# Kernel tuning notes

Measured on AMD Instinct MI355X. Metric: run time of the kernel, lower is better.

## Reference

```python
import jax, jax.numpy as jnp
import numpy as np

B, S, D = 8, 2048, 512
EPS = 1e-6
ROPE_THETA = 10000.0


def setup_inputs() -> dict:
    key = jax.random.key(0)
    ks = jax.random.split(key, 8)
    scale = 0.02
    return {
        "x": jax.random.normal(ks[0], (B, S, D), dtype=jnp.float32),
        "conv_w": jax.random.normal(ks[1], (D, D, 3), dtype=jnp.float32) * scale,
        "conv_b": jnp.zeros((D,), dtype=jnp.float32),
        "pre_g": jnp.ones((D,), dtype=jnp.float32),
        "q_g": jnp.ones((D,), dtype=jnp.float32),
        "k_g": jnp.ones((D,), dtype=jnp.float32),
        "Wq": jax.random.normal(ks[2], (D, D), dtype=jnp.float32) * scale,
        "Wk": jax.random.normal(ks[3], (D, D), dtype=jnp.float32) * scale,
        "Wv": jax.random.normal(ks[4], (D, D), dtype=jnp.float32) * scale,
    }


def _rmsnorm(x, g, eps=EPS):
    ms = jnp.mean(jnp.square(x), axis=-1, keepdims=True)
    return x * jax.lax.rsqrt(ms + eps) * g


def _rope_tables(seq_len, head_dim, dtype=jnp.float32):
    inv = 1.0 / (ROPE_THETA ** (jnp.arange(0, head_dim, 2, dtype=dtype) / head_dim))
    freqs = jnp.arange(seq_len, dtype=dtype)[:, None] * inv[None, :]  # [S, D/2]
    return jnp.cos(freqs), jnp.sin(freqs)


def _apply_rope(x, cos, sin):
    # x: [B, S, D]; treat last dim as D/2 complex pairs (interleaved real/imag)
    b, s, d = x.shape
    xr = x.reshape(b, s, d // 2, 2)
    x0, x1 = xr[..., 0], xr[..., 1]
    c = cos[None, :, :]
    sn = sin[None, :, :]
    o0 = x0 * c - x1 * sn
    o1 = x0 * sn + x1 * c
    return jnp.stack([o0, o1], axis=-1).reshape(b, s, d)


def reference(x, conv_w, conv_b, pre_g, q_g, k_g, Wq, Wk, Wv):
    b, s, d = x.shape
    # Conv1d over sequence axis (kernel 3, padding 1)
    xc = jnp.transpose(x, (0, 2, 1))  # [B, D, S]
    xc = jax.lax.conv_general_dilated(
        xc, conv_w, window_strides=(1,), padding=[(1, 1)],
        dimension_numbers=("NCH", "OIH", "NCH"))
    xc = xc + conv_b[None, :, None]
    x_norm = _rmsnorm(jnp.transpose(xc, (0, 2, 1)), pre_g)  # [B, S, D]

    q = _rmsnorm(jnp.einsum("bsd,ed->bse", x_norm, Wq), q_g)
    k = _rmsnorm(jnp.einsum("bsd,ed->bse", x_norm, Wk), k_g)
    v = jnp.einsum("bsd,ed->bse", x_norm, Wv)

    cos, sin = _rope_tables(s, d, x.dtype)
    q = _apply_rope(q, cos, sin)
    k = _apply_rope(k, cos, sin)

    scores = jnp.einsum("bqd,bkd->bqk", q, k) / jnp.sqrt(jnp.asarray(d, x.dtype))
    w = jax.nn.softmax(scores, axis=-1)  # dropout is identity in eval mode
    attended = jnp.einsum("bqk,bkd->bqd", w, v)
    out = x + attended
    return out.mean(axis=1)  # [B, D]
```

## Files before the change

### kernel.cpp

```cpp
#include <hip/hip_runtime.h>
#include <math.h>

#define BB 8
#define SS 2048
#define DDIM 512
#define KC 1536
#define EPSV 1e-6f
#define SCALE 0.044194173824159216f
#define LDP  40
#define LDP2 72

typedef unsigned short ushort_t;
using short8 = __attribute__((ext_vector_type(8))) short;
using f32x4  = __attribute__((ext_vector_type(4))) float;

__device__ inline unsigned short f2bf(float f) {
    union { float f; unsigned int u; } v; v.f = f;
    unsigned int r = v.u + 0x7FFFu + ((v.u >> 16) & 1u);
    return (unsigned short)(r >> 16);
}
__device__ inline unsigned int packbf(float a, float b) {
    return (unsigned int)f2bf(a) | ((unsigned int)f2bf(b) << 16);
}
__device__ inline float bf2f(unsigned short s) {
    union { unsigned int u; float f; } v; v.u = ((unsigned int)s) << 16; return v.f;
}
__device__ inline short8 ldfrag(const ushort_t* s, int row, int ko) {
    return *reinterpret_cast<const short8*>(&s[row * LDP + ko]);
}
__device__ inline short8 ldfrag2(const ushort_t* s, int row, int ko) {
    return *reinterpret_cast<const short8*>(&s[row * LDP2 + ko]);
}
__device__ inline uint4 lda_bc(const ushort_t* Ag, int s_, int ko) {
    return (s_ >= 0 && s_ < SS) ? *reinterpret_cast<const uint4*>(&Ag[(size_t)s_ * DDIM + ko])
                                : make_uint4(0, 0, 0, 0);
}

__global__ __launch_bounds__(256) void kx_cast(const float* __restrict__ x,
                                               ushort_t* __restrict__ xbf,
                                               float* __restrict__ xsum)
{
    const int t = threadIdx.x;
    const int b = blockIdx.y;
    const int r0 = blockIdx.x * 16;
    const int c0 = 2 * t;
    float s0 = 0.f, s1 = 0.f;
    for (int r = 0; r < 16; r++) {
        size_t row = (size_t)b * SS + r0 + r;
        float2 v = *reinterpret_cast<const float2*>(&x[row * DDIM + c0]);
        s0 += v.x; s1 += v.y;
        *reinterpret_cast<unsigned int*>(&xbf[row * DDIM + c0]) = packbf(v.x, v.y);
    }
    atomicAdd(&xsum[b * DDIM + c0], s0);
    atomicAdd(&xsum[b * DDIM + c0 + 1], s1);
}

__global__ __launch_bounds__(256) void k0_prep(
    const float* __restrict__ conv_w, const float* __restrict__ Wq,
    const float* __restrict__ Wk, const float* __restrict__ Wv,
    ushort_t* __restrict__ wcat, ushort_t* __restrict__ wqkv)
{
    int idx = blockIdx.x * 256 + threadIdx.x;
    {
        int o = idx / KC, kk = idx - o * KC;
        int t = kk >> 9, i = kk & 511;
        wcat[idx] = f2bf(conv_w[(size_t)o * KC + i * 3 + t]);
    }
    {
        int n = idx >> 9, d = idx & 511;
        const float* src = (n < 512) ? &Wq[(size_t)n * DDIM + d]
                         : (n < 1024) ? &Wk[(size_t)(n - 512) * DDIM + d]
                         : &Wv[(size_t)(n - 1024) * DDIM + d];
        wqkv[idx] = f2bf(*src);
    }
}

__global__ __launch_bounds__(256) void k1b_conv(
    const ushort_t* __restrict__ xbf, const ushort_t* __restrict__ wcat,
    const float* __restrict__ conv_b, ushort_t* __restrict__ ybf, float* __restrict__ rs)
{
    __shared__ ushort_t As[128 * LDP2];
    __shared__ ushort_t Bs[128 * LDP2];
    const int t = threadIdx.x;
    const int lane = t & 63, w = t >> 6;
    const int lm = lane & 15, lq = lane >> 4;
    const int wm = w >> 1, wn = w & 1;
    const int sr = t >> 3, sc = (t & 7) * 8;
    const int s0 = blockIdx.x * 128;
    const int n0 = blockIdx.y * 128;
    const int b  = blockIdx.z;
    const ushort_t* Ag = xbf + (size_t)b * SS * DDIM;
    const ushort_t* Bg = wcat + (size_t)n0 * KC;

    f32x4 acc[4][4];
    #pragma unroll
    for (int i = 0; i < 4; i++)
        #pragma unroll
        for (int j = 0; j < 4; j++) acc[i][j] = (f32x4){0.f, 0.f, 0.f, 0.f};

    uint4 ra0, ra1, ra2, ra3, rb0, rb1, rb2, rb3;
    #define LOADAB(dc) { \
        int tg_ = (dc) >> 3, ko_ = ((dc) & 7) * 64 + sc, kb_ = (dc) * 64 + sc; \
        int sa_ = s0 + sr + tg_ - 1; \
        ra0 = lda_bc(Ag, sa_,      ko_); ra1 = lda_bc(Ag, sa_ + 32, ko_); \
        ra2 = lda_bc(Ag, sa_ + 64, ko_); ra3 = lda_bc(Ag, sa_ + 96, ko_); \
        rb0 = *reinterpret_cast<const uint4*>(&Bg[(size_t)sr * KC + kb_]); \
        rb1 = *reinterpret_cast<const uint4*>(&Bg[(size_t)(sr + 32) * KC + kb_]); \
        rb2 = *reinterpret_cast<const uint4*>(&Bg[(size_t)(sr + 64) * KC + kb_]); \
        rb3 = *reinterpret_cast<const uint4*>(&Bg[(size_t)(sr + 96) * KC + kb_]); }

    LOADAB(0);
    for (int dc = 0; dc < 24; dc++) {
        *reinterpret_cast<uint4*>(&As[(sr)      * LDP2 + sc]) = ra0;
        *reinterpret_cast<uint4*>(&As[(sr + 32) * LDP2 + sc]) = ra1;
        *reinterpret_cast<uint4*>(&As[(sr + 64) * LDP2 + sc]) = ra2;
        *reinterpret_cast<uint4*>(&As[(sr + 96) * LDP2 + sc]) = ra3;
        *reinterpret_cast<uint4*>(&Bs[(sr)      * LDP2 + sc]) = rb0;
        *reinterpret_cast<uint4*>(&Bs[(sr + 32) * LDP2 + sc]) = rb1;
        *reinterpret_cast<uint4*>(&Bs[(sr + 64) * LDP2 + sc]) = rb2;
        *reinterpret_cast<uint4*>(&Bs[(sr + 96) * LDP2 + sc]) = rb3;
        __syncthreads();
        if (dc < 23) LOADAB(dc + 1);
        #pragma unroll
        for (int half = 0; half < 2; half++) {
            short8 af0 = ldfrag2(As, wm * 64 +  0 + lm, half * 32 + lq * 8);
            short8 af1 = ldfrag2(As, wm * 64 + 16 + lm, half * 32 + lq * 8);
            short8 af2 = ldfrag2(As, wm * 64 + 32 + lm, half * 32 + lq * 8);
            short8 af3 = ldfrag2(As, wm * 64 + 48 + lm, half * 32 + lq * 8);
            #pragma unroll
            for (int nt = 0; nt < 4; nt++) {
                short8 bfv = ldfrag2(Bs, wn * 64 + nt * 16 + lm, half * 32 + lq * 8);
                acc[0][nt] = __builtin_amdgcn_mfma_f32_16x16x32_bf16(af0, bfv, acc[0][nt], 0, 0, 0);
                acc[1][nt] = __builtin_amdgcn_mfma_f32_16x16x32_bf16(af1, bfv, acc[1][nt], 0, 0, 0);
                acc[2][nt] = __builtin_amdgcn_mfma_f32_16x16x32_bf16(af2, bfv, acc[2][nt], 0, 0, 0);
                acc[3][nt] = __builtin_amdgcn_mfma_f32_16x16x32_bf16(af3, bfv, acc[3][nt], 0, 0, 0);
            }
        }
        __syncthreads();
    }
    #undef LOADAB

    const int rbase = s0 + wm * 64;
    const int cbase = n0 + wn * 64;
    ushort_t* yb = ybf + (size_t)b * SS * DDIM;
    float* rsb = rs + (size_t)b * SS;
    float bias[4];
    #pragma unroll
    for (int nt = 0; nt < 4; nt++) bias[nt] = conv_b[cbase + nt * 16 + lm];
    #pragma unroll
    for (int mt = 0; mt < 4; mt++) {
        float pr[4] = {0.f, 0.f, 0.f, 0.f};
        #pragma unroll
        for (int nt = 0; nt < 4; nt++) {
            #pragma unroll
            for (int r = 0; r < 4; r++) {
                float val = acc[mt][nt][r] + bias[nt];
                yb[(size_t)(rbase + mt * 16 + lq * 4 + r) * DDIM + cbase + nt * 16 + lm] = f2bf(val);
                pr[r] = fmaf(val, val, pr[r]);
            }
        }
        #pragma unroll
        for (int r = 0; r < 4; r++) {
            float p = pr[r];
            p += __shfl_xor(p, 1, 64); p += __shfl_xor(p, 2, 64);
            p += __shfl_xor(p, 4, 64); p += __shfl_xor(p, 8, 64);
            if (lm == 0) atomicAdd(&rsb[rbase + mt * 16 + lq * 4 + r], p);
        }
    }
}

__global__ __launch_bounds__(256) void k1n_norm(
    const ushort_t* __restrict__ ybf, const float* __restrict__ rs,
    const float* __restrict__ pre_g, ushort_t* __restrict__ xnbf)
{
    const int t = threadIdx.x;
    const int b = blockIdx.y;
    const int r0 = blockIdx.x * 8;
    float2 pg = *reinterpret_cast<const float2*>(&pre_g[2 * t]);
    for (int r = 0; r < 8; r++) {
        size_t row = (size_t)b * SS + r0 + r;
        float inv = rsqrtf(rs[row] * (1.0f / DDIM) + EPSV);
        unsigned int yv = *reinterpret_cast<const unsigned int*>(&ybf[row * DDIM + 2 * t]);
        float v0 = bf2f((ushort_t)(yv & 0xFFFF)), v1 = bf2f((ushort_t)(yv >> 16));
        *reinterpret_cast<unsigned int*>(&xnbf[row * DDIM + 2 * t]) =
            packbf(v0 * inv * pg.x, v1 * inv * pg.y);
    }
}

__global__ __launch_bounds__(256) void k1c_qkv(
    const ushort_t* __restrict__ xnbf, const ushort_t* __restrict__ wqkv,
    ushort_t* __restrict__ qraw, ushort_t* __restrict__ kraw, ushort_t* __restrict__ vb,
    float* __restrict__ rq, float* __restrict__ rk)
{
    __shared__ ushort_t As[128 * LDP2];
    __shared__ ushort_t Bs[128 * LDP2];
    const int t = threadIdx.x;
    const int lane = t & 63, w = t >> 6;
    const int lm = lane & 15, lq = lane >> 4;
    const int wm = w >> 1, wn = w & 1;
    const int sr = t >> 3, sc = (t & 7) * 8;
    const int s0 = blockIdx.x * 128;
    const int n0 = blockIdx.y * 128;
    const int b  = blockIdx.z;
    const ushort_t* Ag = xnbf + ((size_t)b * SS + s0) * DDIM;
    const ushort_t* Bg = wqkv + (size_t)n0 * DDIM;

    f32x4 acc[4][4];
    #pragma unroll
    for (int i = 0; i < 4; i++)
        #pragma unroll
        for (int j = 0; j < 4; j++) acc[i][j] = (f32x4){0.f, 0.f, 0.f, 0.f};

    uint4 ra0, ra1, ra2, ra3, rb0, rb1, rb2, rb3;
    #define LOADAB2(dc) { \
        int ko_ = (dc) * 64 + sc; \
        ra0 = *reinterpret_cast<const uint4*>(&Ag[(size_t)sr * DDIM + ko_]); \
        ra1 = *reinterpret_cast<const uint4*>(&Ag[(size_t)(sr + 32) * DDIM + ko_]); \
        ra2 = *reinterpret_cast<const uint4*>(&Ag[(size_t)(sr + 64) * DDIM + ko_]); \
        ra3 = *reinterpret_cast<const uint4*>(&Ag[(size_t)(sr + 96) * DDIM + ko_]); \
        rb0 = *reinterpret_cast<const uint4*>(&Bg[(size_t)sr * DDIM + ko_]); \
        rb1 = *reinterpret_cast<const uint4*>(&Bg[(size_t)(sr + 32) * DDIM + ko_]); \
        rb2 = *reinterpret_cast<const uint4*>(&Bg[(size_t)(sr + 64) * DDIM + ko_]); \
        rb3 = *reinterpret_cast<const uint4*>(&Bg[(size_t)(sr + 96) * DDIM + ko_]); }

    LOADAB2(0);
    for (int dc = 0; dc < 8; dc++) {
        *reinterpret_cast<uint4*>(&As[(sr)      * LDP2 + sc]) = ra0;
        *reinterpret_cast<uint4*>(&As[(sr + 32) * LDP2 + sc]) = ra1;
        *reinterpret_cast<uint4*>(&As[(sr + 64) * LDP2 + sc]) = ra2;
        *reinterpret_cast<uint4*>(&As[(sr + 96) * LDP2 + sc]) = ra3;
        *reinterpret_cast<uint4*>(&Bs[(sr)      * LDP2 + sc]) = rb0;
        *reinterpret_cast<uint4*>(&Bs[(sr + 32) * LDP2 + sc]) = rb1;
        *reinterpret_cast<uint4*>(&Bs[(sr + 64) * LDP2 + sc]) = rb2;
        *reinterpret_cast<uint4*>(&Bs[(sr + 96) * LDP2 + sc]) = rb3;
        __syncthreads();
        if (dc < 7) LOADAB2(dc + 1);
        #pragma unroll
        for (int half = 0; half < 2; half++) {
            short8 af0 = ldfrag2(As, wm * 64 +  0 + lm, half * 32 + lq * 8);
            short8 af1 = ldfrag2(As, wm * 64 + 16 + lm, half * 32 + lq * 8);
            short8 af2 = ldfrag2(As, wm * 64 + 32 + lm, half * 32 + lq * 8);
            short8 af3 = ldfrag2(As, wm * 64 + 48 + lm, half * 32 + lq * 8);
            #pragma unroll
            for (int nt = 0; nt < 4; nt++) {
                short8 bfv = ldfrag2(Bs, wn * 64 + nt * 16 + lm, half * 32 + lq * 8);
                acc[0][nt] = __builtin_amdgcn_mfma_f32_16x16x32_bf16(af0, bfv, acc[0][nt], 0, 0, 0);
                acc[1][nt] = __builtin_amdgcn_mfma_f32_16x16x32_bf16(af1, bfv, acc[1][nt], 0, 0, 0);
                acc[2][nt] = __builtin_amdgcn_mfma_f32_16x16x32_bf16(af2, bfv, acc[2][nt], 0, 0, 0);
                acc[3][nt] = __builtin_amdgcn_mfma_f32_16x16x32_bf16(af3, bfv, acc[3][nt], 0, 0, 0);
            }
        }
        __syncthreads();
    }
    #undef LOADAB2

    const int which = blockIdx.y >> 2;
    const int rbase = s0 + wm * 64;
    const int cbase = ((blockIdx.y & 3) * 128) + wn * 64;
    if (which == 2) {
        ushort_t* vbb = vb + (size_t)b * SS * DDIM;
        #pragma unroll
        for (int mt = 0; mt < 4; mt++)
            #pragma unroll
            for (int nt = 0; nt < 4; nt++)
                #pragma unroll
                for (int r = 0; r < 4; r++)
                    vbb[(size_t)(rbase + mt * 16 + lq * 4 + r) * DDIM + cbase + nt * 16 + lm] =
                        f2bf(acc[mt][nt][r]);
    } else {
        ushort_t* db = (which ? kraw : qraw) + (size_t)b * SS * DDIM;
        float* rb = (which ? rk : rq) + (size_t)b * SS;
        #pragma unroll
        for (int mt = 0; mt < 4; mt++) {
            float pr[4] = {0.f, 0.f, 0.f, 0.f};
            #pragma unroll
            for (int nt = 0; nt < 4; nt++) {
                #pragma unroll
                for (int r = 0; r < 4; r++) {
                    float val = acc[mt][nt][r];
                    db[(size_t)(rbase + mt * 16 + lq * 4 + r) * DDIM + cbase + nt * 16 + lm] = f2bf(val);
                    pr[r] = fmaf(val, val, pr[r]);
                }
            }
            #pragma unroll
            for (int r = 0; r < 4; r++) {
                float p = pr[r];
                p += __shfl_xor(p, 1, 64); p += __shfl_xor(p, 2, 64);
                p += __shfl_xor(p, 4, 64); p += __shfl_xor(p, 8, 64);
                if (lm == 0) atomicAdd(&rb[rbase + mt * 16 + lq * 4 + r], p);
            }
        }
    }
}

__global__ __launch_bounds__(256) void k1d_rope(
    ushort_t* q_io, ushort_t* k_io,
    const float* __restrict__ rq, const float* __restrict__ rk,
    const float* __restrict__ q_g, const float* __restrict__ k_g)
{
    const int t = threadIdx.x;
    const int b = blockIdx.y;
    const int r0 = blockIdx.x * 8;
    const int c0 = 2 * t;
    float qg0 = q_g[c0], qg1 = q_g[c0 + 1];
    float kg0 = k_g[c0], kg1 = k_g[c0 + 1];
    float invf = (float)pow(10000.0, -(double)c0 / (double)DDIM);
    for (int r = 0; r < 8; r++) {
        int srow = r0 + r;
        size_t rowi = (size_t)b * SS + srow;
        float iq = rsqrtf(rq[rowi] * (1.0f / DDIM) + EPSV);
        float ik = rsqrtf(rk[rowi] * (1.0f / DDIM) + EPSV);
        size_t off = rowi * DDIM + c0;
        unsigned int qv = *reinterpret_cast<const unsigned int*>(&q_io[off]);
        unsigned int kv = *reinterpret_cast<const unsigned int*>(&k_io[off]);
        float q0 = bf2f((ushort_t)(qv & 0xFFFF)) * iq * qg0;
        float q1 = bf2f((ushort_t)(qv >> 16)) * iq * qg1;
        float k0v = bf2f((ushort_t)(kv & 0xFFFF)) * ik * kg0;
        float k1v = bf2f((ushort_t)(kv >> 16)) * ik * kg1;
        float ang = (float)srow * invf, sn, cs;
        sincosf(ang, &sn, &cs);
        *reinterpret_cast<unsigned int*>(&q_io[off]) = packbf(q0 * cs - q1 * sn, q0 * sn + q1 * cs);
        *reinterpret_cast<unsigned int*>(&k_io[off]) = packbf(k0v * cs - k1v * sn, k0v * sn + k1v * cs);
    }
}

__global__ __launch_bounds__(256, 4) void k2a_rowsum(
    const ushort_t* __restrict__ qb, const ushort_t* __restrict__ kb,
    ushort_t* __restrict__ P, float* __restrict__ l)
{
    __shared__ ushort_t As[128 * LDP];
    __shared__ ushort_t Bs[128 * LDP];
    const int t = threadIdx.x;
    const int lane = t & 63, w = t >> 6;
    const int lm = lane & 15, lq = lane >> 4;
    const int wm = w >> 1, wn = w & 1;
    const int srow = t >> 2, scol = (t & 3) * 8;
    const int b  = blockIdx.x;
    const int qt = blockIdx.y;
    const int kt = blockIdx.z;

    const ushort_t* Ag = qb + ((size_t)b * SS + qt * 128) * DDIM;
    const ushort_t* Bg = kb + ((size_t)b * SS + kt * 128) * DDIM;

    f32x4 acc[4][4];
    #pragma unroll
    for (int i = 0; i < 4; i++)
        #pragma unroll
        for (int j = 0; j < 4; j++) acc[i][j] = (f32x4){0.f, 0.f, 0.f, 0.f};

    uint4 ra0 = *reinterpret_cast<const uint4*>(&Ag[(size_t)srow * DDIM + scol]);
    uint4 ra1 = *reinterpret_cast<const uint4*>(&Ag[(size_t)(srow + 64) * DDIM + scol]);
    uint4 rb0 = *reinterpret_cast<const uint4*>(&Bg[(size_t)srow * DDIM + scol]);
    uint4 rb1 = *reinterpret_cast<const uint4*>(&Bg[(size_t)(srow + 64) * DDIM + scol]);

    for (int dc = 0; dc < 16; dc++) {
        *reinterpret_cast<uint4*>(&As[srow * LDP + scol]) = ra0;
        *reinterpret_cast<uint4*>(&As[(srow + 64) * LDP + scol]) = ra1;
        *reinterpret_cast<uint4*>(&Bs[srow * LDP + scol]) = rb0;
        *reinterpret_cast<uint4*>(&Bs[(srow + 64) * LDP + scol]) = rb1;
        __syncthreads();
        if (dc < 15) {
            int off = (dc + 1) * 32 + scol;
            ra0 = *reinterpret_cast<const uint4*>(&Ag[(size_t)srow * DDIM + off]);
            ra1 = *reinterpret_cast<const uint4*>(&Ag[(size_t)(srow + 64) * DDIM + off]);
            rb0 = *reinterpret_cast<const uint4*>(&Bg[(size_t)srow * DDIM + off]);
            rb1 = *reinterpret_cast<const uint4*>(&Bg[(size_t)(srow + 64) * DDIM + off]);
        }
        short8 af[4];
        #pragma unroll
        for (int mt = 0; mt < 4; mt++)
            af[mt] = ldfrag(As, wm * 64 + mt * 16 + lm, lq * 8);
        #pragma unroll
        for (int nt = 0; nt < 4; nt++) {
            short8 bfv = ldfrag(Bs, wn * 64 + nt * 16 + lm, lq * 8);
            #pragma unroll
            for (int mt = 0; mt < 4; mt++)
                acc[mt][nt] = __builtin_amdgcn_mfma_f32_16x16x32_bf16(af[mt], bfv, acc[mt][nt], 0, 0, 0);
        }
        __syncthreads();
    }

    const int rbase = qt * 128 + wm * 64;
    const int cbase = kt * 128 + wn * 64;
    ushort_t* Pb = P + (size_t)b * SS * SS;
    float* lrow = l + (size_t)b * SS;
    #pragma unroll
    for (int mt = 0; mt < 4; mt++) {
        #pragma unroll
        for (int r = 0; r < 4; r++) {
            const int row = rbase + mt * 16 + lq * 4 + r;
            float rowp = 0.f;
            #pragma unroll
            for (int nt = 0; nt < 4; nt++) {
                float e = __expf(acc[mt][nt][r] * SCALE);
                Pb[(size_t)row * SS + cbase + nt * 16 + lm] = f2bf(e);
                rowp += e;
            }
            float p = rowp;
            p += __shfl_xor(p, 1, 64); p += __shfl_xor(p, 2, 64);
            p += __shfl_xor(p, 4, 64); p += __shfl_xor(p, 8, 64);
            if (lm == 0) atomicAdd(&lrow[row], p);
        }
    }
}

__global__ __launch_bounds__(256) void k2c_colred(
    const ushort_t* __restrict__ P, const float* __restrict__ l,
    float* __restrict__ cw)
{
    const int t = threadIdx.x;
    const int b = blockIdx.z;
    const int k0 = blockIdx.x * 1024 + t * 4;
    const int q0 = blockIdx.y * 128;
    const ushort_t* Pb = P + ((size_t)b * SS + q0) * SS;
    const float* lb = l + (size_t)b * SS + q0;
    float a0 = 0.f, a1 = 0.f, a2 = 0.f, a3 = 0.f;
    for (int q = 0; q < 128; q++) {
        float rl = 1.0f / lb[q];
        uint2 pp = *reinterpret_cast<const uint2*>(&Pb[(size_t)q * SS + k0]);
        a0 = fmaf(bf2f((ushort_t)(pp.x & 0xFFFF)), rl, a0);
        a1 = fmaf(bf2f((ushort_t)(pp.x >> 16)), rl, a1);
        a2 = fmaf(bf2f((ushort_t)(pp.y & 0xFFFF)), rl, a2);
        a3 = fmaf(bf2f((ushort_t)(pp.y >> 16)), rl, a3);
    }
    atomicAdd(&cw[(size_t)b * SS + k0], a0);
    atomicAdd(&cw[(size_t)b * SS + k0 + 1], a1);
    atomicAdd(&cw[(size_t)b * SS + k0 + 2], a2);
    atomicAdd(&cw[(size_t)b * SS + k0 + 3], a3);
}

__global__ __launch_bounds__(256) void k4_out(
    const float* __restrict__ xsum, const ushort_t* __restrict__ v,
    const float* __restrict__ cwv, float* __restrict__ out)
{
    const int b = blockIdx.x, c = blockIdx.y;
    const int t = threadIdx.x;
    const int srow0 = c * (SS / 16);
    const ushort_t* vb = v + ((size_t)b * SS + srow0) * DDIM;
    const float* cwb   = cwv + (size_t)b * SS + srow0;
    float a0 = (c == 0) ? xsum[b * DDIM + t]       : 0.f;
    float a1 = (c == 0) ? xsum[b * DDIM + t + 256] : 0.f;
    for (int r = 0; r < SS / 16; r++) {
        float w = cwb[r];
        a0 += w * bf2f(vb[(size_t)r * DDIM + t]);
        a1 += w * bf2f(vb[(size_t)r * DDIM + t + 256]);
    }
    atomicAdd(&out[b * DDIM + t],       a0 * (1.0f / SS));
    atomicAdd(&out[b * DDIM + t + 256], a1 * (1.0f / SS));
}

extern "C" void kernel_launch(void* const* d_in, const int* in_sizes, int n_in,
                              void* d_out, int out_size, void* d_ws, size_t ws_size,
                              hipStream_t stream)
{
    const float* x      = (const float*)d_in[0];
    const float* conv_w = (const float*)d_in[1];
    const float* conv_b = (const float*)d_in[2];
    const float* pre_g  = (const float*)d_in[3];
    const float* q_g    = (const float*)d_in[4];
    const float* k_g    = (const float*)d_in[5];
    const float* Wq     = (const float*)d_in[6];
    const float* Wk     = (const float*)d_in[7];
    const float* Wv     = (const float*)d_in[8];
    float* out          = (float*)d_out;

    const size_t NTOK = (size_t)BB * SS * DDIM;
    char* p = (char*)d_ws;
    ushort_t* xbf = (ushort_t*)p; p += NTOK * 2;
    ushort_t* ybf = (ushort_t*)p; p += NTOK * 2;
    ushort_t* xn  = (ushort_t*)p; p += NTOK * 2;
                         p += NTOK * 2;
    ushort_t* qio = (ushort_t*)p; p += NTOK * 2;
    ushort_t* kio = (ushort_t*)p; p += NTOK * 2;
    ushort_t* vb  = (ushort_t*)p; p += NTOK * 2;
    ushort_t* wcat = (ushort_t*)p; p += (size_t)DDIM * KC * 2;
    ushort_t* wqkv = (ushort_t*)p; p += (size_t)KC * DDIM * 2;
    float* rs   = (float*)p; p += (size_t)BB * SS * 4;
    float* rq   = (float*)p; p += (size_t)BB * SS * 4;
    float* rk   = (float*)p; p += (size_t)BB * SS * 4;
    float* lbuf = (float*)p; p += (size_t)BB * SS * 4;
    float* cwb  = (float*)p; p += (size_t)BB * SS * 4;
    float* xsum = (float*)p; p += (size_t)BB * DDIM * 4;

    ushort_t* Pbuf = xbf;

    (void)hipMemsetAsync(d_out, 0, (size_t)out_size * sizeof(float), stream);
    (void)hipMemsetAsync(rs, 0, ((size_t)BB * SS * 5 + (size_t)BB * DDIM) * sizeof(float), stream);

    kx_cast<<<dim3(SS / 16, BB), 256, 0, stream>>>(x, xbf, xsum);
    k0_prep<<<dim3(DDIM * KC / 256), 256, 0, stream>>>(conv_w, Wq, Wk, Wv, wcat, wqkv);
    k1b_conv<<<dim3(SS / 128, 4, BB), 256, 0, stream>>>(xbf, wcat, conv_b, ybf, rs);
    k1n_norm<<<dim3(SS / 8, BB), 256, 0, stream>>>(ybf, rs, pre_g, xn);
    k1c_qkv<<<dim3(SS / 128, 12, BB), 256, 0, stream>>>(xn, wqkv, qio, kio, vb, rq, rk);
    k1d_rope<<<dim3(SS / 8, BB), 256, 0, stream>>>(qio, kio, rq, rk, q_g, k_g);
    k2a_rowsum<<<dim3(BB, SS / 128, SS / 128), 256, 0, stream>>>(qio, kio, Pbuf, lbuf);
    k2c_colred<<<dim3(SS / 1024, SS / 128, BB), 256, 0, stream>>>(Pbuf, lbuf, cwb);
    k4_out<<<dim3(BB, 16), 256, 0, stream>>>(xsum, vb, cwb, out);
}
```

Measured before the change: 283.8 us.

## Widen QK^T tile to 256 keys, vectorize cast and column-reduction kernels

The scores kernel now computes a 128x256 tile per block, reusing each Q fragment across two key halves and halving the number of Q reloads and row-sum atomics. Its occupancy hint is dropped because the accumulator count doubles. The column-reduction kernel switches to 16-byte loads with 8 columns per thread over 64-row query chunks. The cast kernel uses float4 loads and combines its two row halves in shared memory before issuing atomics. The larger tile raises register pressure and may lower occupancy.

```diff
diff --git a/kernel.cpp b/kernel.cpp
--- a/kernel.cpp
+++ b/kernel.cpp
@@ -40,19 +40,32 @@
                                                ushort_t* __restrict__ xbf,
                                                float* __restrict__ xsum)
 {
+    __shared__ float xr[512];
     const int t = threadIdx.x;
     const int b = blockIdx.y;
-    const int r0 = blockIdx.x * 16;
-    const int c0 = 2 * t;
-    float s0 = 0.f, s1 = 0.f;
-    for (int r = 0; r < 16; r++) {
+    const int half = t >> 7;
+    const int c0 = (t & 127) * 4;
+    const int r0 = blockIdx.x * 16 + half * 8;
+    float s0 = 0.f, s1 = 0.f, s2 = 0.f, s3 = 0.f;
+    for (int r = 0; r < 8; r++) {
         size_t row = (size_t)b * SS + r0 + r;
-        float2 v = *reinterpret_cast<const float2*>(&x[row * DDIM + c0]);
-        s0 += v.x; s1 += v.y;
-        *reinterpret_cast<unsigned int*>(&xbf[row * DDIM + c0]) = packbf(v.x, v.y);
-    }
-    atomicAdd(&xsum[b * DDIM + c0], s0);
-    atomicAdd(&xsum[b * DDIM + c0 + 1], s1);
+        float4 v = *reinterpret_cast<const float4*>(&x[row * DDIM + c0]);
+        s0 += v.x; s1 += v.y; s2 += v.z; s3 += v.w;
+        *reinterpret_cast<uint2*>(&xbf[row * DDIM + c0]) =
+            make_uint2(packbf(v.x, v.y), packbf(v.z, v.w));
+    }
+    if (half) {
+        float4* dst = reinterpret_cast<float4*>(&xr[(t - 128) * 4]);
+        *dst = make_float4(s0, s1, s2, s3);
+    }
+    __syncthreads();
+    if (!half) {
+        float4 o = *reinterpret_cast<const float4*>(&xr[t * 4]);
+        atomicAdd(&xsum[b * DDIM + c0],     s0 + o.x);
+        atomicAdd(&xsum[b * DDIM + c0 + 1], s1 + o.y);
+        atomicAdd(&xsum[b * DDIM + c0 + 2], s2 + o.z);
+        atomicAdd(&xsum[b * DDIM + c0 + 3], s3 + o.w);
+    }
 }
 
 __global__ __launch_bounds__(256) void k0_prep(
@@ -324,12 +337,12 @@
     }
 }
 
-__global__ __launch_bounds__(256, 4) void k2a_rowsum(
+__global__ __launch_bounds__(256) void k2a_rowsum(
     const ushort_t* __restrict__ qb, const ushort_t* __restrict__ kb,
     ushort_t* __restrict__ P, float* __restrict__ l)
 {
     __shared__ ushort_t As[128 * LDP];
-    __shared__ ushort_t Bs[128 * LDP];
+    __shared__ ushort_t Bs[256 * LDP];
     const int t = threadIdx.x;
     const int lane = t & 63, w = t >> 6;
     const int lm = lane & 15, lq = lane >> 4;
@@ -340,48 +353,63 @@
     const int kt = blockIdx.z;
 
     const ushort_t* Ag = qb + ((size_t)b * SS + qt * 128) * DDIM;
-    const ushort_t* Bg = kb + ((size_t)b * SS + kt * 128) * DDIM;
-
-    f32x4 acc[4][4];
+    const ushort_t* Bg = kb + ((size_t)b * SS + kt * 256) * DDIM;
+
+    f32x4 accA[4][4], accB[4][4];
     #pragma unroll
     for (int i = 0; i < 4; i++)
         #pragma unroll
-        for (int j = 0; j < 4; j++) acc[i][j] = (f32x4){0.f, 0.f, 0.f, 0.f};
-
-    uint4 ra0 = *reinterpret_cast<const uint4*>(&Ag[(size_t)srow * DDIM + scol]);
-    uint4 ra1 = *reinterpret_cast<const uint4*>(&Ag[(size_t)(srow + 64) * DDIM + scol]);
-    uint4 rb0 = *reinterpret_cast<const uint4*>(&Bg[(size_t)srow * DDIM + scol]);
-    uint4 rb1 = *reinterpret_cast<const uint4*>(&Bg[(size_t)(srow + 64) * DDIM + scol]);
-
+        for (int j = 0; j < 4; j++) {
+            accA[i][j] = (f32x4){0.f, 0.f, 0.f, 0.f};
+            accB[i][j] = (f32x4){0.f, 0.f, 0.f, 0.f};
+        }
+
+    uint4 qa0, qa1, kb0, kb1, kb2, kb3;
+    #define LOADQK(dc) { \
+        int ko_ = (dc) * 32 + scol; \
+        qa0 = *reinterpret_cast<const uint4*>(&Ag[(size_t)srow * DDIM + ko_]); \
+        qa1 = *reinterpret_cast<const uint4*>(&Ag[(size_t)(srow + 64) * DDIM + ko_]); \
+        kb0 = *reinterpret_cast<const uint4*>(&Bg[(size_t)srow * DDIM + ko_]); \
+        kb1 = *reinterpret_cast<const uint4*>(&Bg[(size_t)(srow + 64) * DDIM + ko_]); \
+        kb2 = *reinterpret_cast<const uint4*>(&Bg[(size_t)(srow + 128) * DDIM + ko_]); \
+        kb3 = *reinterpret_cast<const uint4*>(&Bg[(size_t)(srow + 192) * DDIM + ko_]); }
+
+    LOADQK(0);
     for (int dc = 0; dc < 16; dc++) {
-        *reinterpret_cast<uint4*>(&As[srow * LDP + scol]) = ra0;
-        *reinterpret_cast<uint4*>(&As[(srow + 64) * LDP + scol]) = ra1;
-        *reinterpret_cast<uint4*>(&Bs[srow * LDP + scol]) = rb0;
-        *reinterpret_cast<uint4*>(&Bs[(srow + 64) * LDP + scol]) = rb1;
+        *reinterpret_cast<uint4*>(&As[srow * LDP + scol]) = qa0;
+        *reinterpret_cast<uint4*>(&As[(srow + 64) * LDP + scol]) = qa1;
+        *reinterpret_cast<uint4*>(&Bs[srow * LDP + scol]) = kb0;
+        *reinterpret_cast<uint4*>(&Bs[(srow + 64) * LDP + scol]) = kb1;
+        *reinterpret_cast<uint4*>(&Bs[(srow + 128) * LDP + scol]) = kb2;
+        *reinterpret_cast<uint4*>(&Bs[(srow + 192) * LDP + scol]) = kb3;
         __syncthreads();
-        if (dc < 15) {
-            int off = (dc + 1) * 32 + scol;
-            ra0 = *reinterpret_cast<const uint4*>(&Ag[(size_t)srow * DDIM + off]);
-            ra1 = *reinterpret_cast<const uint4*>(&Ag[(size_t)(srow + 64) * DDIM + off]);
-            rb0 = *reinterpret_cast<const uint4*>(&Bg[(size_t)srow * DDIM + off]);
-            rb1 = *reinterpret_cast<const uint4*>(&Bg[(size_t)(srow + 64) * DDIM + off]);
-        }
-        short8 af[4];
-        #pragma unroll
-        for (int mt = 0; mt < 4; mt++)
-            af[mt] = ldfrag(As, wm * 64 + mt * 16 + lm, lq * 8);
+        if (dc < 15) LOADQK(dc + 1);
+        short8 af0 = ldfrag(As, wm * 64 +  0 + lm, lq * 8);
+        short8 af1 = ldfrag(As, wm * 64 + 16 + lm, lq * 8);
+        short8 af2 = ldfrag(As, wm * 64 + 32 + lm, lq * 8);
+        short8 af3 = ldfrag(As, wm * 64 + 48 + lm, lq * 8);
         #pragma unroll
         for (int nt = 0; nt < 4; nt++) {
             short8 bfv = ldfrag(Bs, wn * 64 + nt * 16 + lm, lq * 8);
-            #pragma unroll
-            for (int mt = 0; mt < 4; mt++)
-                acc[mt][nt] = __builtin_amdgcn_mfma_f32_16x16x32_bf16(af[mt], bfv, acc[mt][nt], 0, 0, 0);
+            accA[0][nt] = __builtin_amdgcn_mfma_f32_16x16x32_bf16(af0, bfv, accA[0][nt], 0, 0, 0);
+            accA[1][nt] = __builtin_amdgcn_mfma_f32_16x16x32_bf16(af1, bfv, accA[1][nt], 0, 0, 0);
+            accA[2][nt] = __builtin_amdgcn_mfma_f32_16x16x32_bf16(af2, bfv, accA[2][nt], 0, 0, 0);
+            accA[3][nt] = __builtin_amdgcn_mfma_f32_16x16x32_bf16(af3, bfv, accA[3][nt], 0, 0, 0);
+        }
+        #pragma unroll
+        for (int nt = 0; nt < 4; nt++) {
+            short8 bfv = ldfrag(Bs, 128 + wn * 64 + nt * 16 + lm, lq * 8);
+            accB[0][nt] = __builtin_amdgcn_mfma_f32_16x16x32_bf16(af0, bfv, accB[0][nt], 0, 0, 0);
+            accB[1][nt] = __builtin_amdgcn_mfma_f32_16x16x32_bf16(af1, bfv, accB[1][nt], 0, 0, 0);
+            accB[2][nt] = __builtin_amdgcn_mfma_f32_16x16x32_bf16(af2, bfv, accB[2][nt], 0, 0, 0);
+            accB[3][nt] = __builtin_amdgcn_mfma_f32_16x16x32_bf16(af3, bfv, accB[3][nt], 0, 0, 0);
         }
         __syncthreads();
     }
+    #undef LOADQK
 
     const int rbase = qt * 128 + wm * 64;
-    const int cbase = kt * 128 + wn * 64;
+    const int cbase = kt * 256 + wn * 64;
     ushort_t* Pb = P + (size_t)b * SS * SS;
     float* lrow = l + (size_t)b * SS;
     #pragma unroll
@@ -392,8 +420,14 @@
             float rowp = 0.f;
             #pragma unroll
             for (int nt = 0; nt < 4; nt++) {
-                float e = __expf(acc[mt][nt][r] * SCALE);
+                float e = __expf(accA[mt][nt][r] * SCALE);
                 Pb[(size_t)row * SS + cbase + nt * 16 + lm] = f2bf(e);
+                rowp += e;
+            }
+            #pragma unroll
+            for (int nt = 0; nt < 4; nt++) {
+                float e = __expf(accB[mt][nt][r] * SCALE);
+                Pb[(size_t)row * SS + cbase + 128 + nt * 16 + lm] = f2bf(e);
                 rowp += e;
             }
             float p = rowp;
@@ -409,24 +443,27 @@
     float* __restrict__ cw)
 {
     const int t = threadIdx.x;
-    const int b = blockIdx.z;
-    const int k0 = blockIdx.x * 1024 + t * 4;
-    const int q0 = blockIdx.y * 128;
+    const int b = blockIdx.y;
+    const int k0 = t * 8;
+    const int q0 = blockIdx.x * 64;
     const ushort_t* Pb = P + ((size_t)b * SS + q0) * SS;
     const float* lb = l + (size_t)b * SS + q0;
-    float a0 = 0.f, a1 = 0.f, a2 = 0.f, a3 = 0.f;
-    for (int q = 0; q < 128; q++) {
+    float a[8] = {0.f, 0.f, 0.f, 0.f, 0.f, 0.f, 0.f, 0.f};
+    for (int q = 0; q < 64; q++) {
         float rl = 1.0f / lb[q];
-        uint2 pp = *reinterpret_cast<const uint2*>(&Pb[(size_t)q * SS + k0]);
-        a0 = fmaf(bf2f((ushort_t)(pp.x & 0xFFFF)), rl, a0);
-        a1 = fmaf(bf2f((ushort_t)(pp.x >> 16)), rl, a1);
-        a2 = fmaf(bf2f((ushort_t)(pp.y & 0xFFFF)), rl, a2);
-        a3 = fmaf(bf2f((ushort_t)(pp.y >> 16)), rl, a3);
-    }
-    atomicAdd(&cw[(size_t)b * SS + k0], a0);
-    atomicAdd(&cw[(size_t)b * SS + k0 + 1], a1);
-    atomicAdd(&cw[(size_t)b * SS + k0 + 2], a2);
-    atomicAdd(&cw[(size_t)b * SS + k0 + 3], a3);
+        uint4 pp = *reinterpret_cast<const uint4*>(&Pb[(size_t)q * SS + k0]);
+        a[0] = fmaf(bf2f((ushort_t)(pp.x & 0xFFFF)), rl, a[0]);
+        a[1] = fmaf(bf2f((ushort_t)(pp.x >> 16)), rl, a[1]);
+        a[2] = fmaf(bf2f((ushort_t)(pp.y & 0xFFFF)), rl, a[2]);
+        a[3] = fmaf(bf2f((ushort_t)(pp.y >> 16)), rl, a[3]);
+        a[4] = fmaf(bf2f((ushort_t)(pp.z & 0xFFFF)), rl, a[4]);
+        a[5] = fmaf(bf2f((ushort_t)(pp.z >> 16)), rl, a[5]);
+        a[6] = fmaf(bf2f((ushort_t)(pp.w & 0xFFFF)), rl, a[6]);
+        a[7] = fmaf(bf2f((ushort_t)(pp.w >> 16)), rl, a[7]);
+    }
+    #pragma unroll
+    for (int i = 0; i < 8; i++)
+        atomicAdd(&cw[(size_t)b * SS + k0 + i], a[i]);
 }
 
 __global__ __launch_bounds__(256) void k4_out(
@@ -493,7 +530,7 @@
     k1n_norm<<<dim3(SS / 8, BB), 256, 0, stream>>>(ybf, rs, pre_g, xn);
     k1c_qkv<<<dim3(SS / 128, 12, BB), 256, 0, stream>>>(xn, wqkv, qio, kio, vb, rq, rk);
     k1d_rope<<<dim3(SS / 8, BB), 256, 0, stream>>>(qio, kio, rq, rk, q_g, k_g);
-    k2a_rowsum<<<dim3(BB, SS / 128, SS / 128), 256, 0, stream>>>(qio, kio, Pbuf, lbuf);
-    k2c_colred<<<dim3(SS / 1024, SS / 128, BB), 256, 0, stream>>>(Pbuf, lbuf, cwb);
+    k2a_rowsum<<<dim3(BB, SS / 128, SS / 256), 256, 0, stream>>>(qio, kio, Pbuf, lbuf);
+    k2c_colred<<<dim3(SS / 64, BB), 256, 0, stream>>>(Pbuf, lbuf, cwb);
     k4_out<<<dim3(BB, 16), 256, 0, stream>>>(xsum, vb, cwb, out);
 }
```

After: 298.3 us. 1.05x slower.
